# Kernel optimization log

Measured on AMD Instinct MI355X. Metric: run time of the kernel, lower is better.

Reference implementation:

```python
import jax, jax.numpy as jnp
import numpy as np

B, H, W, C = 4, 128, 128, 180
HEADS, WS = 6, 16
HID = 720            # int(dim * mlp_ratio)
CONV_SCALE = 0.01
N = WS * WS          # tokens per window
CM = C // 2          # CAB mid channels (is_light_sr -> compress_ratio=2)
CS = C // 30         # channel-attention squeeze channels


def conv2d(x, w, b=None, padding=0, dilation=1, groups=1):
    out = jax.lax.conv_general_dilated(
        x, w, (1, 1), [(padding, padding), (padding, padding)],
        rhs_dilation=(dilation, dilation),
        dimension_numbers=('NCHW', 'OIHW', 'NCHW'),
        feature_group_count=groups)
    if b is not None:
        out = out + b[None, :, None, None]
    return out


def layernorm(x, g, b, eps=1e-5):
    mu = jnp.mean(x, -1, keepdims=True)
    var = jnp.var(x, -1, keepdims=True)
    return (x - mu) * jax.lax.rsqrt(var + eps) * g + b


def make_rpi(ws):
    coords = np.stack(np.meshgrid(np.arange(ws), np.arange(ws), indexing='ij'))
    cf = coords.reshape(2, -1)
    rel = (cf[:, :, None] - cf[:, None, :]).transpose(1, 2, 0).astype(np.int64)
    rel[:, :, 0] += ws - 1
    rel[:, :, 1] += ws - 1
    rel[:, :, 0] *= 2 * ws - 1
    return rel.sum(-1)  # [n, n]


def _forward(rpi_sa, x, norm1_g, norm1_b, rpb_table, qkv_w, qkv_b, proj_w, proj_b,
             cab_w0, cab_b0, cab_w1, cab_b1, cab_w2, cab_b2, cab_w3, cab_b3,
             ca_w1, ca_b1, ca_w2, ca_b2, norm2_g, norm2_b,
             fc1_w, fc1_b, dw_w, dw_b, pw_w, pw_b, sa_w, fc2_w, fc2_b):
    b = x.shape[0]
    shortcut = x
    xn = layernorm(x, norm1_g, norm1_b)
    x_img = xn.reshape(b, H, W, C)

    # --- window partition (shift_size=0 -> no roll, no mask) ---
    xw = x_img.reshape(b, H // WS, WS, W // WS, WS, C)
    xw = xw.transpose(0, 1, 3, 2, 4, 5).reshape(-1, N, C)  # [b*nW, n, C]

    # --- window attention with relative position bias ---
    hd = C // HEADS
    qkv = (xw @ qkv_w.T + qkv_b).reshape(-1, N, 3, HEADS, hd)
    qkv = qkv.transpose(2, 0, 3, 1, 4)  # [3, b*nW, heads, n, hd]
    q, k, v = qkv[0], qkv[1], qkv[2]
    attn = jnp.einsum('whnd,whmd->whnm', q * (hd ** -0.5), k)
    bias = rpb_table[rpi_sa.reshape(-1)].reshape(N, N, HEADS).transpose(2, 0, 1)
    attn = jax.nn.softmax(attn + bias[None], axis=-1)
    out = jnp.einsum('whnm,whmd->whnd', attn, v)
    out = out.transpose(0, 2, 1, 3).reshape(-1, N, C)
    out = out @ proj_w.T + proj_b

    # --- window reverse ---
    attn_x = out.reshape(b, H // WS, W // WS, WS, WS, C)
    attn_x = attn_x.transpose(0, 1, 3, 2, 4, 5).reshape(b, H * W, C)

    # --- CAB conv branch on norm1 output (light-SR variant) ---
    x2d = x_img.transpose(0, 3, 1, 2)  # NCHW
    y = conv2d(x2d, cab_w0, cab_b0)                                  # 1x1 C->C/2
    y = conv2d(y, cab_w1, cab_b1, padding=1, groups=CM)              # dw 3x3
    y = jax.nn.gelu(y, approximate=False)
    y = conv2d(y, cab_w2, cab_b2)                                    # 1x1 C/2->C
    y = conv2d(y, cab_w3, cab_b3, padding=2, dilation=2, groups=C)   # dw 3x3 dil2
    a = jnp.mean(y, (2, 3), keepdims=True)                           # GAP
    a = jax.nn.relu(conv2d(a, ca_w1, ca_b1))
    a = jax.nn.sigmoid(conv2d(a, ca_w2, ca_b2))
    conv_x = (y * a).transpose(0, 2, 3, 1).reshape(b, H * W, C)

    x = shortcut + attn_x + conv_x * CONV_SCALE

    # --- DSConvAttnFFN ---
    xn2 = layernorm(x, norm2_g, norm2_b)
    hdn = jax.nn.gelu(xn2 @ fc1_w.T + fc1_b, approximate=False)
    h2d = hdn.reshape(b, H, W, HID).transpose(0, 3, 1, 2)
    h2d = jax.nn.relu(conv2d(h2d, dw_w, dw_b, padding=1, groups=HID))
    h2d = jax.nn.relu(conv2d(h2d, pw_w, pw_b))
    mp = jnp.max(h2d, 1, keepdims=True)
    ap = jnp.mean(h2d, 1, keepdims=True)
    sa = jax.nn.sigmoid(conv2d(jnp.concatenate([mp, ap], 1), sa_w, padding=3))
    h2d = h2d * sa
    hdn = h2d.transpose(0, 2, 3, 1).reshape(b, H * W, HID)
    return x + (hdn @ fc2_w.T + fc2_b)


def setup_inputs():
    key = jax.random.key(0)
    ks = iter(jax.random.split(key, 48))
    def w(*shape):
        return jax.random.normal(next(ks), shape, jnp.float32) * 0.02
    return dict(
        x=jax.random.normal(next(ks), (B, H * W, C), jnp.float32),
        x_size_h=H, x_size_w=W,
        rpi_sa=jnp.asarray(make_rpi(WS)),
        norm1_g=jnp.ones((C,), jnp.float32), norm1_b=jnp.zeros((C,), jnp.float32),
        rpb_table=w((2 * WS - 1) ** 2, HEADS),
        qkv_w=w(3 * C, C), qkv_b=jnp.zeros((3 * C,), jnp.float32),
        proj_w=w(C, C), proj_b=jnp.zeros((C,), jnp.float32),
        cab_w0=w(CM, C, 1, 1), cab_b0=jnp.zeros((CM,), jnp.float32),
        cab_w1=w(CM, 1, 3, 3), cab_b1=jnp.zeros((CM,), jnp.float32),
        cab_w2=w(C, CM, 1, 1), cab_b2=jnp.zeros((C,), jnp.float32),
        cab_w3=w(C, 1, 3, 3), cab_b3=jnp.zeros((C,), jnp.float32),
        ca_w1=w(CS, C, 1, 1), ca_b1=jnp.zeros((CS,), jnp.float32),
        ca_w2=w(C, CS, 1, 1), ca_b2=jnp.zeros((C,), jnp.float32),
        norm2_g=jnp.ones((C,), jnp.float32), norm2_b=jnp.zeros((C,), jnp.float32),
        fc1_w=w(HID, C), fc1_b=jnp.zeros((HID,), jnp.float32),
        dw_w=w(HID, 1, 3, 3), dw_b=jnp.zeros((HID,), jnp.float32),
        pw_w=w(HID, HID, 1, 1), pw_b=jnp.zeros((HID,), jnp.float32),
        sa_w=w(1, 2, 7, 7),
        fc2_w=w(C, HID), fc2_b=jnp.zeros((C,), jnp.float32),
    )


def reference(x, x_size_h, x_size_w, rpi_sa, norm1_g, norm1_b, rpb_table,
              qkv_w, qkv_b, proj_w, proj_b,
              cab_w0, cab_b0, cab_w1, cab_b1, cab_w2, cab_b2, cab_w3, cab_b3,
              ca_w1, ca_b1, ca_w2, ca_b2, norm2_g, norm2_b,
              fc1_w, fc1_b, dw_w, dw_b, pw_w, pw_b, sa_w, fc2_w, fc2_b):
    del x_size_h, x_size_w  # fixed to H, W
    return _forward(rpi_sa, x, norm1_g, norm1_b, rpb_table, qkv_w, qkv_b,
                    proj_w, proj_b, cab_w0, cab_b0, cab_w1, cab_b1, cab_w2,
                    cab_b2, cab_w3, cab_b3, ca_w1, ca_b1, ca_w2, ca_b2,
                    norm2_g, norm2_b, fc1_w, fc1_b, dw_w, dw_b, pw_w, pw_b,
                    sa_w, fc2_w, fc2_b)
```

## Files before the change

### kernel.cpp

```cpp
#include <hip/hip_runtime.h>
#include <math.h>

#define HH 128
#define WW 128
#define CC 180
#define BB 4
#define IMG (HH*WW)
#define NTOK (BB*IMG)
#define HALFTOK (2*IMG)
#define NHEADS 6
#define HD 30
#define WSZ 16
#define NTOKW (WSZ*WSZ)
#define HID 720
#define QKVSTR 672

typedef __attribute__((ext_vector_type(8))) short short8v;
typedef __attribute__((ext_vector_type(4))) short short4v;
typedef __attribute__((ext_vector_type(4))) float f32x4;
typedef unsigned short ushortw;

__device__ __forceinline__ float warp_sum(float v) {
    #pragma unroll
    for (int o = 32; o > 0; o >>= 1) v += __shfl_xor(v, o);
    return v;
}
__device__ __forceinline__ float warp_max(float v) {
    #pragma unroll
    for (int o = 32; o > 0; o >>= 1) v = fmaxf(v, __shfl_xor(v, o));
    return v;
}
__device__ __forceinline__ float gelu_exact(float v) {
    return 0.5f * v * (1.f + erff(v * 0.70710678118654752f));
}
__device__ __forceinline__ ushortw f2bf(float f) {
    union { float f; unsigned int u; } c; c.f = f;
    unsigned int r = (c.u + 0x7FFFu + ((c.u >> 16) & 1u)) >> 16;
    return (ushortw)r;
}
__device__ __forceinline__ float bf2f(ushortw u) {
    union { unsigned int u; float f; } c; c.u = ((unsigned int)u) << 16; return c.f;
}

__global__ __launch_bounds__(256) void prep_kernel(
    const float* __restrict__ qkv_w, const float* __restrict__ proj_w,
    const float* __restrict__ cab_w0, const float* __restrict__ cab_b0,
    const float* __restrict__ cab_w2,
    const float* __restrict__ fc1_w, const float* __restrict__ pw_w,
    const float* __restrict__ fc2_w,
    const float* __restrict__ cab_w1, const float* __restrict__ cab_b1,
    const float* __restrict__ cab_w3, const float* __restrict__ cab_b3,
    const float* __restrict__ dw_w, const float* __restrict__ dw_b,
    const float* __restrict__ qkv_b, const int* __restrict__ rpi,
    const float* __restrict__ rpb,
    ushortw* __restrict__ wqkvc, ushortw* __restrict__ wproj,
    ushortw* __restrict__ wcab2,
    ushortw* __restrict__ wfc1, ushortw* __restrict__ wpw, ushortw* __restrict__ wfc2,
    float* __restrict__ dwt1, float* __restrict__ db1,
    float* __restrict__ dwt2, float* __restrict__ db2,
    float* __restrict__ dwt3, float* __restrict__ db3,
    float* __restrict__ qb672, float* __restrict__ biasN)
{
    int idx = blockIdx.x * 256 + threadIdx.x;
    if (idx < 129024) {
        int r = idx / 192, k = idx - r * 192;
        float v = 0.f;
        if (r < 576) {
            int sub = r / 192, rem = r - sub * 192;
            int hh = rem >> 5, dd = rem & 31;
            if (dd < 30 && k < 180) v = qkv_w[(sub * 180 + hh * 30 + dd) * 180 + k];
        } else if (r < 666) {
            if (k < 180) v = cab_w0[(r - 576) * 180 + k];
        }
        wqkvc[idx] = f2bf(v);
    } else if (idx < 178176) {
        int l = idx - 129024; int r = l / 192, k = l - r * 192;
        wproj[l] = f2bf((r < 180 && k < 180) ? proj_w[r * 180 + k] : 0.f);
    } else if (idx < 210944) {
        int l = idx - 178176; int r = l / 128, k = l - r * 128;
        wcab2[l] = f2bf((r < 180 && k < 90) ? cab_w2[r * 90 + k] : 0.f);
    } else if (idx < 358400) {
        int l = idx - 210944; int r = l / 192, k = l - r * 192;
        wfc1[l] = f2bf((r < 720 && k < 180) ? fc1_w[r * 180 + k] : 0.f);
    } else if (idx < 948224) {
        int l = idx - 358400; int r = l / 768, k = l - r * 768;
        wpw[l] = f2bf((r < 720 && k < 720) ? pw_w[r * 720 + k] : 0.f);
    } else if (idx < 1144832) {
        int l = idx - 948224; int r = l / 768, k = l - r * 768;
        wfc2[l] = f2bf((r < 180 && k < 720) ? fc2_w[r * 720 + k] : 0.f);
    } else if (idx < 1145984) {
        int l = idx - 1144832; int c = l / 9, k = l - c * 9;
        dwt1[k * 128 + c] = (c < 90) ? cab_w1[c * 9 + k] : 0.f;
        if (k == 0) db1[c] = (c < 90) ? cab_b1[c] : 0.f;
    } else if (idx < 1147712) {
        int l = idx - 1145984; int c = l / 9, k = l - c * 9;
        dwt2[k * 192 + c] = (c < 180) ? cab_w3[c * 9 + k] : 0.f;
        if (k == 0) db2[c] = (c < 180) ? cab_b3[c] : 0.f;
    } else if (idx < 1154624) {
        int l = idx - 1147712; int c = l / 9, k = l - c * 9;
        dwt3[k * 768 + c] = (c < 720) ? dw_w[c * 9 + k] : 0.f;
        if (k == 0) db3[c] = (c < 720) ? dw_b[c] : 0.f;
    } else if (idx < 1155296) {
        int l = idx - 1154624;
        float v = 0.f;
        if (l < 576) {
            int sub = l / 192, rem = l - sub * 192;
            int hh = rem >> 5, dd = rem & 31;
            if (dd < 30) v = qkv_b[sub * 180 + hh * 30 + dd];
        } else if (l < 666) {
            v = cab_b0[l - 576];
        }
        qb672[l] = v;
    } else if (idx < 1220832) {
        int l = idx - 1155296;
        int r = rpi[l];
        #pragma unroll
        for (int h = 0; h < NHEADS; h++)
            biasN[((size_t)h << 16) + l] = rpb[r * NHEADS + h];
    }
}

__global__ __launch_bounds__(256) void ln_kernel(
    const float* __restrict__ x, const float* __restrict__ g,
    const float* __restrict__ b, ushortw* __restrict__ out, ushortw* __restrict__ xb)
{
    int wid = threadIdx.x >> 6, lane = threadIdx.x & 63;
    int t = blockIdx.x * 4 + wid;
    size_t off = (size_t)t * CC;
    size_t off2 = (size_t)t * 192;
    bool has2 = lane < (CC - 128);
    float v0 = x[off + lane];
    float v1 = x[off + lane + 64];
    float v2 = has2 ? x[off + lane + 128] : 0.f;
    xb[off + lane] = f2bf(v0);
    xb[off + lane + 64] = f2bf(v1);
    if (has2) xb[off + lane + 128] = f2bf(v2);
    float s = warp_sum(v0 + v1 + v2);
    float mu = s * (1.f / CC);
    float d0 = v0 - mu, d1 = v1 - mu, d2 = has2 ? v2 - mu : 0.f;
    float var = warp_sum(d0*d0 + d1*d1 + d2*d2) * (1.f / CC);
    float rs = rsqrtf(var + 1e-5f);
    out[off2 + lane]      = f2bf(d0 * rs * g[lane]      + b[lane]);
    out[off2 + lane + 64] = f2bf(d1 * rs * g[lane + 64] + b[lane + 64]);
    out[off2 + lane + 128] = has2 ? f2bf(d2 * rs * g[lane + 128] + b[lane + 128]) : (ushortw)0;
}

__global__ __launch_bounds__(256) void mgemm_kernel(
    const ushortw* __restrict__ A, const ushortw* __restrict__ Wt,
    const float* __restrict__ bias, void* __restrict__ Cout,
    int M, int N, int Kp, int ldc, int outbf, int zfill, int act, int residbf, int nN,
    const float* __restrict__ rowscale, const void* __restrict__ residv)
{
    __shared__ ushortw sA[2][128 * 32];
    __shared__ ushortw sB[2][128 * 32];
    int tid = threadIdx.x, lane = tid & 63, wid = tid >> 6;
    int total = (int)gridDim.x;
    int orig = blockIdx.x;
    int q = total >> 3, r = total & 7;
    int xcd = orig & 7, slot = orig >> 3;
    int wgid = (xcd < r ? xcd * (q + 1) : r * (q + 1) + (xcd - r) * q) + slot;
    int mp = wgid / nN, np = wgid - mp * nN;
    int m0 = mp << 7, n0 = np << 7;
    int wm = (wid >> 1) << 6, wn = (wid & 1) << 6;
    int lrow = lane & 15, kgrp = lane >> 4;

    f32x4 acc[4][4];
    #pragma unroll
    for (int i = 0; i < 4; i++)
        #pragma unroll
        for (int j = 0; j < 4; j++)
            #pragma unroll
            for (int rr = 0; rr < 4; rr++) acc[i][j][rr] = 0.f;

    int nk = Kp >> 5;
    #pragma unroll
    for (int qq = 0; qq < 2; qq++) {
        int seg = (wid << 1) + qq;
        int row = (seg << 4) + (lane >> 2);
        int cg = (lane & 3) ^ (row & 3) ^ ((row >> 2) & 3);
        const ushortw* ga = A + (size_t)(m0 + row) * Kp + (cg << 3);
        __builtin_amdgcn_global_load_lds(
            (const __attribute__((address_space(1))) void*)ga,
            (__attribute__((address_space(3))) void*)&sA[0][seg << 9], 16, 0, 0);
        const ushortw* gb = Wt + (size_t)(n0 + row) * Kp + (cg << 3);
        __builtin_amdgcn_global_load_lds(
            (const __attribute__((address_space(1))) void*)gb,
            (__attribute__((address_space(3))) void*)&sB[0][seg << 9], 16, 0, 0);
    }
    __syncthreads();

    int cur = 0;
    for (int t = 0; t < nk; t++) {
        if (t + 1 < nk) {
            int kk2 = (t + 1) << 5;
            #pragma unroll
            for (int qq = 0; qq < 2; qq++) {
                int seg = (wid << 1) + qq;
                int row = (seg << 4) + (lane >> 2);
                int cg = (lane & 3) ^ (row & 3) ^ ((row >> 2) & 3);
                const ushortw* ga = A + (size_t)(m0 + row) * Kp + kk2 + (cg << 3);
                __builtin_amdgcn_global_load_lds(
                    (const __attribute__((address_space(1))) void*)ga,
                    (__attribute__((address_space(3))) void*)&sA[cur ^ 1][seg << 9], 16, 0, 0);
                const ushortw* gb = Wt + (size_t)(n0 + row) * Kp + kk2 + (cg << 3);
                __builtin_amdgcn_global_load_lds(
                    (const __attribute__((address_space(1))) void*)gb,
                    (__attribute__((address_space(3))) void*)&sB[cur ^ 1][seg << 9], 16, 0, 0);
            }
        }
        short8v a[4], b[4];
        #pragma unroll
        for (int i = 0; i < 4; i++) {
            int rr = wm + (i << 4) + lrow;
            int slot2 = kgrp ^ (rr & 3) ^ ((rr >> 2) & 3);
            a[i] = *reinterpret_cast<const short8v*>(&sA[cur][(rr << 5) + (slot2 << 3)]);
        }
        #pragma unroll
        for (int j = 0; j < 4; j++) {
            int rr = wn + (j << 4) + lrow;
            int slot2 = kgrp ^ (rr & 3) ^ ((rr >> 2) & 3);
            b[j] = *reinterpret_cast<const short8v*>(&sB[cur][(rr << 5) + (slot2 << 3)]);
        }
        #pragma unroll
        for (int i = 0; i < 4; i++)
            #pragma unroll
            for (int j = 0; j < 4; j++)
                acc[i][j] = __builtin_amdgcn_mfma_f32_16x16x32_bf16(b[j], a[i], acc[i][j], 0, 0, 0);
        __syncthreads();
        cur ^= 1;
    }
    #pragma unroll
    for (int i = 0; i < 4; i++) {
        int row = m0 + wm + (i << 4) + lrow;
        float rsv = rowscale ? rowscale[row] : 1.f;
        #pragma unroll
        for (int j = 0; j < 4; j++) {
            int colb = n0 + wn + (j << 4) + (kgrp << 2);
            if (colb < N) {
                float4 bi4 = *reinterpret_cast<const float4*>(bias + colb);
                float vv[4];
                vv[0] = acc[i][j][0]; vv[1] = acc[i][j][1];
                vv[2] = acc[i][j][2]; vv[3] = acc[i][j][3];
                if (rowscale) {
                    vv[0] *= rsv; vv[1] *= rsv; vv[2] *= rsv; vv[3] *= rsv;
                }
                vv[0] += bi4.x; vv[1] += bi4.y; vv[2] += bi4.z; vv[3] += bi4.w;
                if (act == 1) {
                    vv[0] = gelu_exact(vv[0]); vv[1] = gelu_exact(vv[1]);
                    vv[2] = gelu_exact(vv[2]); vv[3] = gelu_exact(vv[3]);
                } else if (act == 2) {
                    vv[0] = fmaxf(vv[0], 0.f); vv[1] = fmaxf(vv[1], 0.f);
                    vv[2] = fmaxf(vv[2], 0.f); vv[3] = fmaxf(vv[3], 0.f);
                }
                if (residv) {
                    if (residbf) {
                        short4v rv = *reinterpret_cast<const short4v*>(
                            (const ushortw*)residv + (size_t)row * N + colb);
                        vv[0] += bf2f((ushortw)rv[0]); vv[1] += bf2f((ushortw)rv[1]);
                        vv[2] += bf2f((ushortw)rv[2]); vv[3] += bf2f((ushortw)rv[3]);
                    } else {
                        float4 rv = *reinterpret_cast<const float4*>(
                            (const float*)residv + (size_t)row * N + colb);
                        vv[0] += rv.x; vv[1] += rv.y; vv[2] += rv.z; vv[3] += rv.w;
                    }
                }
                if (outbf) {
                    short4v o;
                    o[0] = (short)f2bf(vv[0]); o[1] = (short)f2bf(vv[1]);
                    o[2] = (short)f2bf(vv[2]); o[3] = (short)f2bf(vv[3]);
                    *reinterpret_cast<short4v*>((ushortw*)Cout + (size_t)row * ldc + colb) = o;
                } else {
                    float4 o = make_float4(vv[0], vv[1], vv[2], vv[3]);
                    *reinterpret_cast<float4*>((float*)Cout + (size_t)row * ldc + colb) = o;
                }
            } else if (zfill && colb < ldc) {
                if (outbf) {
                    short4v o; o[0] = 0; o[1] = 0; o[2] = 0; o[3] = 0;
                    *reinterpret_cast<short4v*>((ushortw*)Cout + (size_t)row * ldc + colb) = o;
                } else {
                    *reinterpret_cast<float4*>((float*)Cout + (size_t)row * ldc + colb) =
                        make_float4(0.f, 0.f, 0.f, 0.f);
                }
            }
        }
    }
}

__global__ __launch_bounds__(256, 3) void attn_mfma_kernel(
    const ushortw* __restrict__ qkvP, const float* __restrict__ biasN,
    ushortw* __restrict__ out)
{
    __shared__ ushortw Vc[32 * 33 * 8];
    __shared__ ushortw Kc[256 * 32];
    __shared__ ushortw Pl[4][2048];
    const float SCALE = 0.18257418583505536f;
    int blk = blockIdx.x;
    int img = blk / 384;
    int rem = blk - img * 384;
    int win = rem / NHEADS;
    int h = rem - win * NHEADS;
    int base = img * IMG + (win >> 3) * WSZ * WW + (win & 7) * WSZ;
    int tid = threadIdx.x;
    int lane = tid & 63, w = tid >> 6;
    int a15 = lane & 15, kg = lane >> 4;

    {
        int j = tid;
        int g = base + (j >> 4) * WW + (j & 15);
        const ushortw* vp = qkvP + (size_t)g * QKVSTR + 384 + h * 32;
        short8v c0 = *reinterpret_cast<const short8v*>(vp);
        short8v c1 = *reinterpret_cast<const short8v*>(vp + 8);
        short8v c2 = *reinterpret_cast<const short8v*>(vp + 16);
        short8v c3 = *reinterpret_cast<const short8v*>(vp + 24);
        int bo = (j >> 3) * 264 + (j & 7);
        #pragma unroll
        for (int e = 0; e < 8; e++)  Vc[bo + (e) * 8]      = (ushortw)c0[e];
        #pragma unroll
        for (int e = 0; e < 8; e++)  Vc[bo + (8 + e) * 8]  = (ushortw)c1[e];
        #pragma unroll
        for (int e = 0; e < 8; e++)  Vc[bo + (16 + e) * 8] = (ushortw)c2[e];
        #pragma unroll
        for (int e = 0; e < 8; e++)  Vc[bo + (24 + e) * 8] = (ushortw)c3[e];
        const ushortw* kp = qkvP + (size_t)g * QKVSTR + 192 + h * 32;
        short8v k0 = *reinterpret_cast<const short8v*>(kp);
        short8v k1 = *reinterpret_cast<const short8v*>(kp + 8);
        short8v k2 = *reinterpret_cast<const short8v*>(kp + 16);
        short8v k3 = *reinterpret_cast<const short8v*>(kp + 24);
        short8v* krow = reinterpret_cast<short8v*>(&Kc[j * 32]);
        int jsw = (j >> 1) & 3;
        krow[0 ^ jsw] = k0; krow[1 ^ jsw] = k1; krow[2 ^ jsw] = k2; krow[3 ^ jsw] = k3;
    }
    __syncthreads();

    ushortw* Pw = &Pl[w][0];
    int xsw = (a15 & 7) << 2;
    f32x4 zf = {0.f, 0.f, 0.f, 0.f};
    #pragma unroll 1
    for (int si = 0; si < 4; si++) {
        int strip = (w << 2) + si;
        short8v qf = *reinterpret_cast<const short8v*>(
            qkvP + (size_t)(base + strip * WW + a15) * QKVSTR + h * 32 + (kg << 3));
        float psum = 0.f;
        f32x4 o0 = zf, o1 = zf;
        const float* brow = biasN + ((size_t)h << 16) + (size_t)((strip << 4) + a15) * 256;
        #pragma unroll
        for (int half = 0; half < 2; half++) {
            float4 b4s[8];
            #pragma unroll
            for (int j8 = 0; j8 < 8; j8++) {
                int jt = (half << 3) + j8;
                b4s[j8] = *reinterpret_cast<const float4*>(brow + (jt << 4) + (kg << 2));
            }
            f32x4 s[8];
            __builtin_amdgcn_s_setprio(1);
            #pragma unroll
            for (int j8 = 0; j8 < 8; j8++) {
                int jt = (half << 3) + j8;
                int row = (jt << 4) + a15;
                short8v ka = reinterpret_cast<const short8v*>(&Kc[row * 32])[kg ^ ((row >> 1) & 3)];
                s[j8] = __builtin_amdgcn_mfma_f32_16x16x32_bf16(ka, qf, zf, 0, 0, 0);
            }
            __builtin_amdgcn_s_setprio(0);
            #pragma unroll
            for (int j8 = 0; j8 < 8; j8++) {
                float p0 = __expf(fmaf(s[j8][0], SCALE, b4s[j8].x));
                float p1 = __expf(fmaf(s[j8][1], SCALE, b4s[j8].y));
                float p2 = __expf(fmaf(s[j8][2], SCALE, b4s[j8].z));
                float p3 = __expf(fmaf(s[j8][3], SCALE, b4s[j8].w));
                psum += (p0 + p1) + (p2 + p3);
                unsigned int u0, u1;
                asm("v_cvt_pk_bf16_f32 %0, %1, %2" : "=v"(u0) : "v"(p0), "v"(p1));
                asm("v_cvt_pk_bf16_f32 %0, %1, %2" : "=v"(u1) : "v"(p2), "v"(p3));
                int dw0 = ((j8 << 3) + (kg << 1)) ^ xsw;
                unsigned long long pk64 = (unsigned long long)u0 | ((unsigned long long)u1 << 32);
                *reinterpret_cast<unsigned long long*>(&Pw[(a15 << 7) + (dw0 << 1)]) = pk64;
            }
            __builtin_amdgcn_s_setprio(1);
            #pragma unroll
            for (int ks4 = 0; ks4 < 4; ks4++) {
                int dwr = ((ks4 << 4) + (kg << 2)) ^ xsw;
                short8v pa = *reinterpret_cast<const short8v*>(&Pw[(a15 << 7) + (dwr << 1)]);
                int kc = (((half << 2) + ks4) << 2) + kg;
                short8v v0 = *reinterpret_cast<const short8v*>(&Vc[(kc * 33 + a15) * 8]);
                short8v v1 = *reinterpret_cast<const short8v*>(&Vc[(kc * 33 + 16 + a15) * 8]);
                o0 = __builtin_amdgcn_mfma_f32_16x16x32_bf16(pa, v0, o0, 0, 0, 0);
                o1 = __builtin_amdgcn_mfma_f32_16x16x32_bf16(pa, v1, o1, 0, 0, 0);
            }
            __builtin_amdgcn_s_setprio(0);
        }
        psum += __shfl_xor(psum, 16);
        psum += __shfl_xor(psum, 32);
        #pragma unroll
        for (int r = 0; r < 4; r++) {
            float pt = __shfl(psum, (kg << 2) + r);
            float inv = 1.f / pt;
            int g = base + strip * WW + (kg << 2) + r;
            ushortw* orow = out + (size_t)g * 192 + h * HD;
            orow[a15] = f2bf(o0[r] * inv);
            if (a15 < 14) orow[16 + a15] = f2bf(o1[r] * inv);
        }
    }
    if (h == 0) {
        for (int idx2 = tid; idx2 < NTOKW * 12; idx2 += 256) {
            int j = idx2 / 12, d = idx2 - (idx2 / 12) * 12;
            int gj = base + (j >> 4) * WW + (j & 15);
            out[(size_t)gj * 192 + 180 + d] = 0;
        }
    }
}

template<int CIN_S, int COP, int OSTR, int DIL, int ACT, int OUTBF>
__global__ __launch_bounds__(256) void dwconv4_kernel(
    const ushortw* __restrict__ in, const float* __restrict__ wt,
    const float* __restrict__ bias, void* __restrict__ out)
{
    constexpr int NC4 = COP >> 2;
    constexpr int NX = 4 + 2 * DIL;
    int idx = blockIdx.x * 256 + threadIdx.x;
    int c4 = idx % NC4;
    int quad = idx / NC4;
    int c = c4 << 2;
    int pix0 = quad << 2;
    int p = pix0 & (IMG - 1);
    int imgbase = pix0 - p;
    int px0 = p & (WW - 1), py = p >> 7;

    float4 w9[9];
    #pragma unroll
    for (int t = 0; t < 9; t++)
        w9[t] = *reinterpret_cast<const float4*>(wt + t * COP + c);
    float4 bi4 = *reinterpret_cast<const float4*>(bias + c);
    float acc[4][4];
    #pragma unroll
    for (int i = 0; i < 4; i++) {
        acc[i][0] = bi4.x; acc[i][1] = bi4.y; acc[i][2] = bi4.z; acc[i][3] = bi4.w;
    }
    #pragma unroll
    for (int ky = 0; ky < 3; ky++) {
        int iy = py + (ky - 1) * DIL;
        if (iy < 0 || iy >= HH) continue;
        const ushortw* rowp = in + (size_t)(imgbase + (iy << 7)) * CIN_S + c;
        #pragma unroll
        for (int xx = 0; xx < NX; xx++) {
            int ix = px0 + xx - DIL;
            if (ix < 0 || ix >= WW) continue;
            short4v v = *reinterpret_cast<const short4v*>(rowp + (size_t)ix * CIN_S);
            float f0 = bf2f((ushortw)v[0]);
            float f1 = bf2f((ushortw)v[1]);
            float f2 = bf2f((ushortw)v[2]);
            float f3 = bf2f((ushortw)v[3]);
            #pragma unroll
            for (int kx = 0; kx < 3; kx++) {
                int i = xx - DIL * kx;
                if (i < 0 || i > 3) continue;
                float4 wv = w9[ky * 3 + kx];
                acc[i][0] = fmaf(f0, wv.x, acc[i][0]);
                acc[i][1] = fmaf(f1, wv.y, acc[i][1]);
                acc[i][2] = fmaf(f2, wv.z, acc[i][2]);
                acc[i][3] = fmaf(f3, wv.w, acc[i][3]);
            }
        }
    }
    if (COP != OSTR && c >= OSTR) return;
    #pragma unroll
    for (int i = 0; i < 4; i++) {
        #pragma unroll
        for (int e = 0; e < 4; e++) {
            float v = acc[i][e];
            if (ACT == 1) v = gelu_exact(v);
            else if (ACT == 2) v = fmaxf(v, 0.f);
            acc[i][e] = v;
        }
        if (OUTBF) {
            short4v o;
            o[0] = (short)f2bf(acc[i][0]); o[1] = (short)f2bf(acc[i][1]);
            o[2] = (short)f2bf(acc[i][2]); o[3] = (short)f2bf(acc[i][3]);
            *reinterpret_cast<short4v*>((ushortw*)out + (size_t)(pix0 + i) * OSTR + c) = o;
        } else {
            float4 o = make_float4(acc[i][0], acc[i][1], acc[i][2], acc[i][3]);
            *reinterpret_cast<float4*>((float*)out + (size_t)(pix0 + i) * OSTR + c) = o;
        }
    }
}

__global__ void gap_kernel(const ushortw* __restrict__ y, float* __restrict__ part)
{
    int blk = blockIdx.x;
    int b = blk >> 7, chunk = blk & 127;
    int c = threadIdx.x;
    if (c >= CC) return;
    size_t basep = ((size_t)b * IMG + (size_t)chunk * 128) * CC;
    float s = 0.f;
    for (int p = 0; p < 128; p++) s += bf2f(y[basep + (size_t)p * CC + c]);
    part[((size_t)b * 128 + chunk) * CC + c] = s;
}

__global__ void ca_kernel(const float* __restrict__ part,
                          const float* __restrict__ w1, const float* __restrict__ b1,
                          const float* __restrict__ w2, const float* __restrict__ b2,
                          float* __restrict__ ca)
{
    __shared__ float gap[BB * CC];
    __shared__ float s1[BB * 6];
    int tid = threadIdx.x;
    for (int idx = tid; idx < BB * CC; idx += 256) {
        int b = idx / CC, c = idx % CC;
        float s = 0.f;
        for (int ch = 0; ch < 128; ch++) s += part[((size_t)b * 128 + ch) * CC + c];
        gap[idx] = s * (1.f / IMG);
    }
    __syncthreads();
    if (tid < BB * 6) {
        int b = tid / 6, cs = tid % 6;
        float s = 0.f;
        for (int c = 0; c < CC; c++) s += w1[cs * CC + c] * gap[b * CC + c];
        s1[tid] = fmaxf(s + b1[cs], 0.f);
    }
    __syncthreads();
    for (int idx = tid; idx < BB * CC; idx += 256) {
        int b = idx / CC, c = idx % CC;
        float s = b2[c];
        #pragma unroll
        for (int cs = 0; cs < 6; cs++) s += w2[c * 6 + cs] * s1[b * 6 + cs];
        ca[idx] = 1.f / (1.f + __expf(-s));
    }
}

__global__ __launch_bounds__(256) void resid_ln_kernel(
    ushortw* __restrict__ x1, const ushortw* __restrict__ y4, const float* __restrict__ ca,
    const float* __restrict__ g, const float* __restrict__ bb,
    ushortw* __restrict__ xn2)
{
    int wid = threadIdx.x >> 6, lane = threadIdx.x & 63;
    int t = blockIdx.x * 4 + wid;
    int b = t >> 14;
    size_t off = (size_t)t * CC;
    size_t off2 = (size_t)t * 192;
    bool has2 = lane < (CC - 128);
    float v0 = bf2f(x1[off+lane])    + 0.01f * bf2f(y4[off+lane])    * ca[b*CC + lane];
    float v1 = bf2f(x1[off+lane+64]) + 0.01f * bf2f(y4[off+lane+64]) * ca[b*CC + lane+64];
    float v2 = 0.f;
    if (has2) v2 = bf2f(x1[off+lane+128]) + 0.01f * bf2f(y4[off+lane+128]) * ca[b*CC + lane+128];
    x1[off+lane] = f2bf(v0); x1[off+lane+64] = f2bf(v1);
    if (has2) x1[off+lane+128] = f2bf(v2);
    float s = warp_sum(v0 + v1 + v2);
    float mu = s * (1.f / CC);
    float d0 = v0-mu, d1 = v1-mu, d2 = has2 ? v2-mu : 0.f;
    float var = warp_sum(d0*d0 + d1*d1 + d2*d2) * (1.f / CC);
    float rs = rsqrtf(var + 1e-5f);
    xn2[off2+lane]      = f2bf(d0 * rs * g[lane]      + bb[lane]);
    xn2[off2+lane+64]   = f2bf(d1 * rs * g[lane+64]   + bb[lane+64]);
    xn2[off2+lane+128]  = has2 ? f2bf(d2 * rs * g[lane+128] + bb[lane+128]) : (ushortw)0;
}

__global__ __launch_bounds__(256) void mpap_kernel(
    const ushortw* __restrict__ h, float* __restrict__ mp, float* __restrict__ ap)
{
    int wid = threadIdx.x >> 6, lane = threadIdx.x & 63;
    int p = blockIdx.x * 4 + wid;
    const ushortw* row = h + (size_t)p * 768;
    float mx = -1e30f, s = 0.f;
    #pragma unroll
    for (int it = 0; it < 3; it++) {
        int j = (lane << 2) + it * 256;
        if (j < HID) {
            short4v v = *reinterpret_cast<const short4v*>(row + j);
            float f0 = bf2f((ushortw)v[0]), f1 = bf2f((ushortw)v[1]);
            float f2 = bf2f((ushortw)v[2]), f3 = bf2f((ushortw)v[3]);
            mx = fmaxf(mx, fmaxf(fmaxf(f0, f1), fmaxf(f2, f3)));
            s += (f0 + f1) + (f2 + f3);
        }
    }
    mx = warp_max(mx); s = warp_sum(s);
    if (lane == 0) { mp[p] = mx; ap[p] = s * (1.f / HID); }
}

__global__ __launch_bounds__(256) void saconv_kernel(
    const float* __restrict__ mp, const float* __restrict__ ap,
    const float* __restrict__ w, float* __restrict__ sa)
{
    __shared__ float smp[22][22];
    __shared__ float sap[22][22];
    int t = blockIdx.x;
    int img = t >> 6;
    int ty = (t >> 3) & 7, tx = t & 7;
    int y0 = ty * 16 - 3, x0 = tx * 16 - 3;
    int tid = threadIdx.x;
    for (int i = tid; i < 22 * 22; i += 256) {
        int ly = i / 22, lx = i - ly * 22;
        int gy = y0 + ly, gx = x0 + lx;
        bool ok = (gy >= 0 && gy < HH && gx >= 0 && gx < WW);
        int pid = img * IMG + gy * WW + gx;
        smp[ly][lx] = ok ? mp[pid] : 0.f;
        sap[ly][lx] = ok ? ap[pid] : 0.f;
    }
    __syncthreads();
    int py = tid >> 4, px = tid & 15;
    float acc = 0.f;
    #pragma unroll
    for (int ky = 0; ky < 7; ky++) {
        #pragma unroll
        for (int kx = 0; kx < 7; kx++) {
            acc += smp[py + ky][px + kx] * w[ky * 7 + kx]
                 + sap[py + ky][px + kx] * w[49 + ky * 7 + kx];
        }
    }
    int p = img * IMG + (ty * 16 + py) * WW + (tx * 16 + px);
    sa[p] = 1.f / (1.f + __expf(-acc));
}

extern "C" void kernel_launch(void* const* d_in, const int* in_sizes, int n_in,
                              void* d_out, int out_size, void* d_ws, size_t ws_size,
                              hipStream_t stream)
{
    const float* x      = (const float*)d_in[0];
    const int*   rpi    = (const int*)d_in[3];
    const float* n1g    = (const float*)d_in[4];
    const float* n1b    = (const float*)d_in[5];
    const float* rpb    = (const float*)d_in[6];
    const float* qkv_w  = (const float*)d_in[7];
    const float* qkv_b  = (const float*)d_in[8];
    const float* proj_w = (const float*)d_in[9];
    const float* proj_b = (const float*)d_in[10];
    const float* cab_w0 = (const float*)d_in[11];
    const float* cab_b0 = (const float*)d_in[12];
    const float* cab_w1 = (const float*)d_in[13];
    const float* cab_b1 = (const float*)d_in[14];
    const float* cab_w2 = (const float*)d_in[15];
    const float* cab_b2 = (const float*)d_in[16];
    const float* cab_w3 = (const float*)d_in[17];
    const float* cab_b3 = (const float*)d_in[18];
    const float* ca_w1  = (const float*)d_in[19];
    const float* ca_b1  = (const float*)d_in[20];
    const float* ca_w2  = (const float*)d_in[21];
    const float* ca_b2  = (const float*)d_in[22];
    const float* n2g    = (const float*)d_in[23];
    const float* n2b    = (const float*)d_in[24];
    const float* fc1_w  = (const float*)d_in[25];
    const float* fc1_b  = (const float*)d_in[26];
    const float* dw_w   = (const float*)d_in[27];
    const float* dw_b   = (const float*)d_in[28];
    const float* pw_w   = (const float*)d_in[29];
    const float* pw_b   = (const float*)d_in[30];
    const float* sa_w   = (const float*)d_in[31];
    const float* fc2_w  = (const float*)d_in[32];
    const float* fc2_b  = (const float*)d_in[33];
    float* outp = (float*)d_out;
    (void)in_sizes; (void)n_in; (void)out_size; (void)ws_size;

    char* ws = (char*)d_ws;
    const size_t S0 = (size_t)NTOK * 192 * 2;
    const size_t S1 = (size_t)NTOK * QKVSTR * 2 + 256;
    const size_t S2 = (size_t)NTOK * 192 * 2;
    const size_t S3 = (size_t)NTOK * 180 * 2;
    const size_t S4 = (size_t)NTOK * 128 * 2;
    const size_t S5 = (size_t)NTOK * 180 * 4;
    char* pA0 = ws;
    char* pA1 = pA0 + S0;
    char* pA2 = pA1 + S1;
    char* pA3 = pA2 + S2;
    char* pA4 = pA3 + S3;
    char* pA5 = pA4 + S4;
    char* tail = pA5 + S5;

    ushortw* xnb    = (ushortw*)pA0;
    ushortw* xn2b   = (ushortw*)pA0;
    ushortw* qkvP   = (ushortw*)pA1;
    ushortw* h1     = (ushortw*)pA1;
    ushortw* h3     = (ushortw*)pA1;
    ushortw* attnbb = (ushortw*)pA2;
    ushortw* y3b    = (ushortw*)pA2;
    ushortw* x1b    = (ushortw*)pA3;
    ushortw* y2b    = (ushortw*)pA4;
    ushortw* h2     = (ushortw*)pA4;
    ushortw* xb     = (ushortw*)pA5;
    ushortw* y4     = (ushortw*)pA5;

    ushortw* wqkvc = (ushortw*)tail;
    ushortw* wproj = wqkvc + 672 * 192;
    ushortw* wcab2 = wproj + 256 * 192;
    ushortw* wfc1  = wcab2 + 256 * 128;
    ushortw* wpw   = wfc1  + 768 * 192;
    ushortw* wfc2  = wpw   + 768 * 768;
    char* tail2 = (char*)(wfc2 + 256 * 768);
    float* dwt1 = (float*)tail2;                 float* db1 = dwt1 + 9*128;
    float* dwt2 = db1 + 128;                     float* db2 = dwt2 + 9*192;
    float* dwt3 = db2 + 192;                     float* db3 = dwt3 + 9*768;
    float* qb672 = db3 + 768;
    char* tail3 = (char*)(qb672 + 672);
    float* biasN = (float*)tail3;
    float* part  = (float*)(tail3 + 1572864);
    float* cabuf = (float*)(tail3 + 1572864 + 393216);
    float* mp    = (float*)(tail3 + 1572864 + 393216 + 4096);
    float* ap    = (float*)(tail3 + 1572864 + 393216 + 4096 + (size_t)HALFTOK * 4);
    float* sab   = (float*)(tail3 + 1572864 + 393216 + 4096 + 2*(size_t)HALFTOK * 4);

    auto gemm = [&](const ushortw* A, const ushortw* Wt, const float* bi, void* Cp,
                    int M, int N, int Kp, int ldc, int outbf, int zfill, int act, int residbf,
                    const float* rs, const void* resid) {
        int nM = M >> 7, nN = (N + 127) >> 7;
        mgemm_kernel<<<dim3(nM * nN), dim3(256), 0, stream>>>(
            A, Wt, bi, Cp, M, N, Kp, ldc, outbf, zfill, act, residbf, nN, rs, resid);
    };

    prep_kernel<<<dim3((1220832 + 255) / 256), dim3(256), 0, stream>>>(
        qkv_w, proj_w, cab_w0, cab_b0, cab_w2, fc1_w, pw_w, fc2_w,
        cab_w1, cab_b1, cab_w3, cab_b3, dw_w, dw_b, qkv_b, rpi, rpb,
        wqkvc, wproj, wcab2, wfc1, wpw, wfc2,
        dwt1, db1, dwt2, db2, dwt3, db3, qb672, biasN);

    ln_kernel<<<dim3(NTOK / 4), dim3(256), 0, stream>>>(x, n1g, n1b, xnb, xb);
    gemm(xnb, wqkvc, qb672, qkvP, NTOK, 672, 192, QKVSTR, 1, 0, 0, 0, nullptr, nullptr);
    attn_mfma_kernel<<<dim3(BB * 64 * NHEADS), dim3(256), 0, stream>>>(qkvP, biasN, attnbb);
    dwconv4_kernel<672, 128, 128, 1, 1, 1><<<dim3(NTOK / 4 * 32 / 256), dim3(256), 0, stream>>>(
        qkvP + 576, dwt1, db1, y2b);
    gemm(attnbb, wproj, proj_b, x1b, NTOK, 180, 192, 180, 1, 0, 0, 1, nullptr, xb);
    gemm(y2b, wcab2, cab_b2, y3b, NTOK, 180, 128, 192, 1, 1, 0, 0, nullptr, nullptr);
    dwconv4_kernel<192, 192, 180, 2, 0, 1><<<dim3(NTOK / 4 * 48 / 256), dim3(256), 0, stream>>>(
        y3b, dwt2, db2, y4);
    gap_kernel<<<dim3(BB * 128), dim3(192), 0, stream>>>(y4, part);
    ca_kernel<<<dim3(1), dim3(256), 0, stream>>>(part, ca_w1, ca_b1, ca_w2, ca_b2, cabuf);
    resid_ln_kernel<<<dim3(NTOK / 4), dim3(256), 0, stream>>>(x1b, y4, cabuf, n2g, n2b, xn2b);
    for (int half = 0; half < 2; half++) {
        size_t toff = (size_t)half * HALFTOK;
        gemm(xn2b + toff * 192, wfc1, fc1_b, h1, HALFTOK, 720, 192, 720, 1, 0, 1, 0, nullptr, nullptr);
        dwconv4_kernel<720, 768, 768, 1, 2, 1><<<dim3(HALFTOK / 4 * 192 / 256), dim3(256), 0, stream>>>(
            h1, dwt3, db3, h2);
        gemm(h2, wpw, pw_b, h3, HALFTOK, 720, 768, 768, 1, 1, 2, 0, nullptr, nullptr);
        mpap_kernel<<<dim3(HALFTOK / 4), dim3(256), 0, stream>>>(h3, mp, ap);
        saconv_kernel<<<dim3(128), dim3(256), 0, stream>>>(mp, ap, sa_w, sab);
        gemm(h3, wfc2, fc2_b, outp + toff * 180, HALFTOK, 180, 768, 180, 0, 0, 0, 1,
             sab, x1b + toff * 180);
    }
}
```

Baseline: 617.4 us.

## Triple-buffer GEMM LDS tiles with explicit vmcnt waits and raw barriers

The bf16 MFMA GEMM kernel moves from double to triple-buffered LDS staging. Global-to-LDS loads for tile t+2 are issued before computing tile t. A partial `s_waitcnt vmcnt(8)` plus a raw `s_barrier` replaces the full `__syncthreads`, so two tiles of loads can stay in flight and hide global memory latency. Per-thread load addresses are also precomputed once instead of every iteration. In exchange, LDS use per block grows from 32KB to 48KB, which may lower occupancy, and correctness now depends on the hand-written wait counts.

```diff
diff --git a/kernel.cpp b/kernel.cpp
--- a/kernel.cpp
+++ b/kernel.cpp
@@ -151,8 +151,8 @@
     int M, int N, int Kp, int ldc, int outbf, int zfill, int act, int residbf, int nN,
     const float* __restrict__ rowscale, const void* __restrict__ residv)
 {
-    __shared__ ushortw sA[2][128 * 32];
-    __shared__ ushortw sB[2][128 * 32];
+    __shared__ ushortw sA[3][128 * 32];
+    __shared__ ushortw sB[3][128 * 32];
     int tid = threadIdx.x, lane = tid & 63, wid = tid >> 6;
     int total = (int)gridDim.x;
     int orig = blockIdx.x;
@@ -173,41 +173,45 @@
             for (int rr = 0; rr < 4; rr++) acc[i][j][rr] = 0.f;
 
     int nk = Kp >> 5;
-    #pragma unroll
-    for (int qq = 0; qq < 2; qq++) {
-        int seg = (wid << 1) + qq;
-        int row = (seg << 4) + (lane >> 2);
-        int cg = (lane & 3) ^ (row & 3) ^ ((row >> 2) & 3);
-        const ushortw* ga = A + (size_t)(m0 + row) * Kp + (cg << 3);
-        __builtin_amdgcn_global_load_lds(
-            (const __attribute__((address_space(1))) void*)ga,
-            (__attribute__((address_space(3))) void*)&sA[0][seg << 9], 16, 0, 0);
-        const ushortw* gb = Wt + (size_t)(n0 + row) * Kp + (cg << 3);
-        __builtin_amdgcn_global_load_lds(
-            (const __attribute__((address_space(1))) void*)gb,
-            (__attribute__((address_space(3))) void*)&sB[0][seg << 9], 16, 0, 0);
-    }
-    __syncthreads();
-
-    int cur = 0;
+    int seg0 = wid << 1;
+    int row0 = (seg0 << 4) + (lane >> 2);
+    int row1 = ((seg0 + 1) << 4) + (lane >> 2);
+    int cg0 = (lane & 3) ^ (row0 & 3) ^ ((row0 >> 2) & 3);
+    int cg1 = (lane & 3) ^ (row1 & 3) ^ ((row1 >> 2) & 3);
+    const ushortw* ga0 = A + (size_t)(m0 + row0) * Kp + (cg0 << 3);
+    const ushortw* ga1 = A + (size_t)(m0 + row1) * Kp + (cg1 << 3);
+    const ushortw* gb0 = Wt + (size_t)(n0 + row0) * Kp + (cg0 << 3);
+    const ushortw* gb1 = Wt + (size_t)(n0 + row1) * Kp + (cg1 << 3);
+
+    #define ISSUE_TILE(slotidx, kk)                                                        \
+        do {                                                                               \
+            __builtin_amdgcn_global_load_lds(                                              \
+                (const __attribute__((address_space(1))) void*)(ga0 + (kk)),               \
+                (__attribute__((address_space(3))) void*)&sA[slotidx][seg0 << 9], 16, 0, 0);\
+            __builtin_amdgcn_global_load_lds(                                              \
+                (const __attribute__((address_space(1))) void*)(gb0 + (kk)),               \
+                (__attribute__((address_space(3))) void*)&sB[slotidx][seg0 << 9], 16, 0, 0);\
+            __builtin_amdgcn_global_load_lds(                                              \
+                (const __attribute__((address_space(1))) void*)(ga1 + (kk)),               \
+                (__attribute__((address_space(3))) void*)&sA[slotidx][(seg0 + 1) << 9], 16, 0, 0);\
+            __builtin_amdgcn_global_load_lds(                                              \
+                (const __attribute__((address_space(1))) void*)(gb1 + (kk)),               \
+                (__attribute__((address_space(3))) void*)&sB[slotidx][(seg0 + 1) << 9], 16, 0, 0);\
+        } while (0)
+
+    ISSUE_TILE(0, 0);
+    if (nk > 1) ISSUE_TILE(1, 32);
+
+    int cur = 0, pre = 2;
     for (int t = 0; t < nk; t++) {
-        if (t + 1 < nk) {
-            int kk2 = (t + 1) << 5;
-            #pragma unroll
-            for (int qq = 0; qq < 2; qq++) {
-                int seg = (wid << 1) + qq;
-                int row = (seg << 4) + (lane >> 2);
-                int cg = (lane & 3) ^ (row & 3) ^ ((row >> 2) & 3);
-                const ushortw* ga = A + (size_t)(m0 + row) * Kp + kk2 + (cg << 3);
-                __builtin_amdgcn_global_load_lds(
-                    (const __attribute__((address_space(1))) void*)ga,
-                    (__attribute__((address_space(3))) void*)&sA[cur ^ 1][seg << 9], 16, 0, 0);
-                const ushortw* gb = Wt + (size_t)(n0 + row) * Kp + kk2 + (cg << 3);
-                __builtin_amdgcn_global_load_lds(
-                    (const __attribute__((address_space(1))) void*)gb,
-                    (__attribute__((address_space(3))) void*)&sB[cur ^ 1][seg << 9], 16, 0, 0);
-            }
-        }
+        if (t + 2 < nk) {
+            ISSUE_TILE(pre, (t + 2) << 5);
+            asm volatile("s_waitcnt vmcnt(8)" ::: "memory");
+        } else {
+            asm volatile("s_waitcnt vmcnt(0)" ::: "memory");
+        }
+        __builtin_amdgcn_s_barrier();
+        asm volatile("" ::: "memory");
         short8v a[4], b[4];
         #pragma unroll
         for (int i = 0; i < 4; i++) {
@@ -226,9 +230,12 @@
             #pragma unroll
             for (int j = 0; j < 4; j++)
                 acc[i][j] = __builtin_amdgcn_mfma_f32_16x16x32_bf16(b[j], a[i], acc[i][j], 0, 0, 0);
-        __syncthreads();
-        cur ^= 1;
-    }
+        asm volatile("" ::: "memory");
+        __builtin_amdgcn_s_barrier();
+        cur = (cur == 2) ? 0 : cur + 1;
+        pre = (pre == 2) ? 0 : pre + 1;
+    }
+    #undef ISSUE_TILE
     #pragma unroll
     for (int i = 0; i < 4; i++) {
         int row = m0 + wm + (i << 4) + lrow;
```

Measured after the change: 612.3 us (median of 2 runs). No clear change (-0.8%).
